# Kernel optimization log

Hardware: AMD Instinct MI355X
Metric: run time of the kernel (lower is better)

## Reference

```python
import jax, jax.numpy as jnp
import numpy as np

B, T, C = 2, 2048, 2048
NH = 16            # query heads
NKV = NH // 2      # kv heads (GQA)
HD = C // NH       # head dim = 128
N_REP = NH // NKV  # 2


def setup_inputs() -> dict:
    key = jax.random.key(0)
    k1, k2, k3 = jax.random.split(key, 3)
    x = jax.random.normal(k1, (B, T, C), jnp.float32)
    w_attn = jax.random.normal(k2, (C, (NH + 2 * NKV) * HD), jnp.float32) * 0.02
    w_proj = jax.random.normal(k3, (C, C), jnp.float32) * 0.02
    t = jnp.arange(T, dtype=jnp.float32)
    inv_freq = 1.0 / (10000.0 ** (jnp.arange(0, HD, 2, dtype=jnp.float32) / HD))
    freqs = t[:, None] * inv_freq[None, :]  # [T, HD//2]
    return {"x": x, "w_attn": w_attn, "w_proj": w_proj,
            "freqs_cos": jnp.cos(freqs), "freqs_sin": jnp.sin(freqs)}


def _rope(v, cos, sin):
    # v: [B, T, H, HD]; complex multiply on (even, odd) pairs
    vr = v.reshape(*v.shape[:-1], HD // 2, 2)
    x0, x1 = vr[..., 0], vr[..., 1]
    c = cos[None, :, None, :]
    s = sin[None, :, None, :]
    o0 = x0 * c - x1 * s
    o1 = x0 * s + x1 * c
    return jnp.stack([o0, o1], axis=-1).reshape(v.shape)


def reference(x, w_attn, w_proj, freqs_cos, freqs_sin):
    qkv = x @ w_attn  # [B, T, (NH+2*NKV)*HD]
    q, k, v = jnp.split(qkv, [NH * HD, (NH + NKV) * HD], axis=-1)
    q = q.reshape(B, T, NH, HD)
    k = k.reshape(B, T, NKV, HD)
    v = v.reshape(B, T, NKV, HD)
    q = _rope(q, freqs_cos, freqs_sin)
    k = _rope(k, freqs_cos, freqs_sin)
    # GQA: group query heads over kv heads instead of repeating k/v
    q = q.transpose(0, 2, 1, 3).reshape(B, NKV, N_REP, T, HD)  # [B, G, R, T, HD]
    k = k.transpose(0, 2, 1, 3)  # [B, G, T, HD]
    v = v.transpose(0, 2, 1, 3)  # [B, G, T, HD]
    scale = jnp.float32(1.0 / np.sqrt(HD))
    scores = jnp.einsum('bgrqd,bgkd->bgrqk', q, k) * scale
    causal = jnp.tril(jnp.ones((T, T), dtype=bool))
    scores = jnp.where(causal, scores, jnp.float32(-1e30))
    p = jax.nn.softmax(scores, axis=-1)
    y = jnp.einsum('bgrqk,bgkd->bgrqd', p, v)  # [B, G, R, T, HD]
    y = y.reshape(B, NH, T, HD).transpose(0, 2, 1, 3).reshape(B, T, C)
    return y @ w_proj
```

## Files before the change

### kernel.cpp

```cpp
#include <hip/hip_runtime.h>
#include <hip/hip_bf16.h>
#include <stdint.h>
#include <stddef.h>

typedef unsigned short u16;
using bf16x8 = __attribute__((ext_vector_type(8))) short;
using f32x4  = __attribute__((ext_vector_type(4))) float;
using f32x16 = __attribute__((ext_vector_type(16))) float;

#define DEVFN static __device__ __forceinline__

DEVFN u16 f2b(float f){ __hip_bfloat16 h = __float2bfloat16(f); return *reinterpret_cast<u16*>(&h); }
DEVFN float b2f(u16 u){ __hip_bfloat16 h; *reinterpret_cast<u16*>(&h) = u; return __bfloat162float(h); }
DEVFN uint32_t pk2(float a, float b){
  uint32_t r; asm("v_cvt_pk_bf16_f32 %0, %1, %2" : "=v"(r) : "v"(a), "v"(b)); return r;
}
DEVFN float ex2(float x){ float r; asm("v_exp_f32 %0, %1" : "=v"(r) : "v"(x)); return r; }

DEVFN void gload_lds16(const void* g, void* l){
  __builtin_amdgcn_global_load_lds(
      (const __attribute__((address_space(1))) void*)g,
      (__attribute__((address_space(3))) void*)l, 16, 0, 0);
}

__global__ void detect_k(const uint32_t* __restrict__ fc_raw, uint32_t* __restrict__ flag){
  if (threadIdx.x == 0 && blockIdx.x == 0)
    flag[0] = (fc_raw[0] == 0x3F800000u) ? 1u : 0u;
}

__global__ __launch_bounds__(256) void cvtf_k(const void* __restrict__ in, float* __restrict__ out,
                                              int n, const uint32_t* __restrict__ flag){
  const int i = blockIdx.x*256 + threadIdx.x;
  if (i >= n) return;
  if (flag[0]) out[i] = ((const float*)in)[i];
  else         out[i] = b2f(((const u16*)in)[i]);
}

__global__ __launch_bounds__(256) void cvtx_k(const void* __restrict__ in, u16* __restrict__ out,
                                              int n8, const uint32_t* __restrict__ flag){
  const int i = blockIdx.x*256 + threadIdx.x;
  if (i >= n8) return;
  __align__(16) u16 e[8];
  if (flag[0]){
    const float* f = (const float*)in + (size_t)i*8;
    float4 a = *(const float4*)f, b = *(const float4*)(f+4);
    e[0]=f2b(a.x); e[1]=f2b(a.y); e[2]=f2b(a.z); e[3]=f2b(a.w);
    e[4]=f2b(b.x); e[5]=f2b(b.y); e[6]=f2b(b.z); e[7]=f2b(b.w);
  } else {
    *(uint4*)e = *((const uint4*)in + i);
  }
  *(uint4*)(out + (size_t)i*8) = *(const uint4*)e;
}

__global__ __launch_bounds__(512) void wtrans_k(const void* __restrict__ in, u16* __restrict__ out,
                                                int C, int R, const uint32_t* __restrict__ flag){
  __shared__ __align__(16) u16 tile[64][72];
  const int r0 = blockIdx.y*64, c0 = blockIdx.x*64;
  const int t = threadIdx.x, r = t>>3, cs = (t&7)*8;
  __align__(16) u16 e[8];
  if (flag[0]){
    const float* f = (const float*)in + (size_t)(r0+r)*C + c0 + cs;
    float4 a = *(const float4*)f, b = *(const float4*)(f+4);
    e[0]=f2b(a.x); e[1]=f2b(a.y); e[2]=f2b(a.z); e[3]=f2b(a.w);
    e[4]=f2b(b.x); e[5]=f2b(b.y); e[6]=f2b(b.z); e[7]=f2b(b.w);
  } else {
    *(uint4*)e = *(const uint4*)((const u16*)in + (size_t)(r0+r)*C + c0 + cs);
  }
#pragma unroll
  for (int j=0;j<8;j++) tile[cs+j][r] = e[j];
  __syncthreads();
  uint4 o = *(const uint4*)&tile[r][cs];
  *(uint4*)(out + (size_t)(c0+r)*R + r0 + cs) = o;
}

__global__ __launch_bounds__(512) void vtrans_k(const u16* __restrict__ qkv, u16* __restrict__ vT){
  __shared__ __align__(16) u16 tile[64][72];
  const int z = blockIdx.z, b = z>>3, g = z&7;
  const u16* in = qkv + (size_t)(b*2048)*4096 + 3072 + g*128;
  u16* out = vT + (size_t)z*128*2048;
  const int r0 = blockIdx.y*64, c0 = blockIdx.x*64;
  const int t = threadIdx.x, r = t>>3, cs = (t&7)*8;
  uint4 v = *(const uint4*)(in + (size_t)(r0+r)*4096 + c0 + cs);
  const u16* e = (const u16*)&v;
#pragma unroll
  for (int j=0;j<8;j++) tile[cs+j][r] = e[j];
  __syncthreads();
  uint4 o = *(const uint4*)&tile[r][cs];
  *(uint4*)(out + (size_t)(c0+r)*2048 + r0 + cs) = o;
}

__global__ __launch_bounds__(256) void rope_k(u16* qkv, const float* __restrict__ fc,
                                              const float* __restrict__ fs){
  const int idx = blockIdx.x*256 + threadIdx.x;
  const int row = idx / 1536;
  const int p   = idx % 1536;
  const int col0 = p*2;
  const int t = row & 2047;
  const int i = p & 63;
  uint32_t* ptr = (uint32_t*)(qkv + (size_t)row*4096 + col0);
  uint32_t u = *ptr;
  float x0 = b2f((u16)(u & 0xffff));
  float x1 = b2f((u16)(u >> 16));
  float c = fc[t*64+i], s = fs[t*64+i];
  float o0 = x0*c - x1*s;
  float o1 = x0*s + x1*c;
  if (col0 < 2048){
    const float S2 = 0.08838834764831845f * 1.4426950408889634f;
    o0 *= S2; o1 *= S2;
  }
  *ptr = (uint32_t)f2b(o0) | ((uint32_t)f2b(o1) << 16);
}

__global__ __launch_bounds__(512) void gemm_p(const u16* __restrict__ A, const u16* __restrict__ Bt,
                                              void* __restrict__ Cv, int M, int N, int K,
                                              const uint32_t* __restrict__ flag, int fin){
  __shared__ __align__(16) u16 L[3*12288];
  const int nwg_x = N>>7;
  int wg = blockIdx.x;
  { const int cpx = (int)gridDim.x >> 3; wg = (wg&7)*cpx + (wg>>3); }
  const int tm = (wg / nwg_x)*256, tn = (wg % nwg_x)*128;
  const int tid = threadIdx.x, w = tid>>6, l = tid&63, lr = l&15, lg = l>>4;
  const int wm = w>>1, wn = w&1;

  f32x4 acc[4][4] = {};

  auto stage = [&](int kt, int buf){
    const int kk = kt*32;
    u16* Lb = &L[buf*12288];
#pragma unroll
    for (int j=0;j<2;j++){
      const int s = j*512 + tid;
      const int row = s>>2, c = s&3;
      const int gch = c ^ ((row ^ (row>>2)) & 3);
      gload_lds16(A + (size_t)(tm + row)*K + kk + gch*8, &Lb[(j*512 + w*64)*8]);
    }
    {
      const int s = tid;
      const int row = s>>2, c = s&3;
      const int gch = c ^ ((row ^ (row>>2)) & 3);
      gload_lds16(Bt + (size_t)(tn + row)*K + kk + gch*8, &Lb[8192 + (w*64)*8]);
    }
  };

  const int nk = K>>5;
  stage(0,0); stage(1,1);
  asm volatile("s_waitcnt vmcnt(3)" ::: "memory");
  __builtin_amdgcn_s_barrier();
  __builtin_amdgcn_sched_barrier(0);

  for (int kt=0; kt<nk; ++kt){
    const int buf = kt % 3;
    if (kt+2 < nk) stage(kt+2, (kt+2) % 3);
    const u16* Ab = &L[buf*12288];
    const u16* Bb = Ab + 8192;
    bf16x8 a[4], b[4];
#pragma unroll
    for (int mi=0;mi<4;mi++){
      const int row = wm*64 + mi*16 + lr;
      a[mi] = *(const bf16x8*)&Ab[row*32 + ((lg ^ ((row ^ (row>>2))&3))*8)];
    }
#pragma unroll
    for (int ni=0;ni<4;ni++){
      const int row = wn*64 + ni*16 + lr;
      b[ni] = *(const bf16x8*)&Bb[row*32 + ((lg ^ ((row ^ (row>>2))&3))*8)];
    }
#pragma unroll
    for (int mi=0;mi<4;mi++)
#pragma unroll
      for (int ni=0;ni<4;ni++)
        acc[mi][ni] = __builtin_amdgcn_mfma_f32_16x16x32_bf16(a[mi], b[ni], acc[mi][ni], 0,0,0);
    __builtin_amdgcn_sched_barrier(0);
    if (kt+2 < nk) asm volatile("s_waitcnt vmcnt(3)" ::: "memory");
    else           asm volatile("s_waitcnt vmcnt(0)" ::: "memory");
    __builtin_amdgcn_s_barrier();
    __builtin_amdgcn_sched_barrier(0);
  }

  const bool of32 = fin && (flag[0] != 0);
#pragma unroll
  for (int mi=0;mi<4;mi++)
#pragma unroll
    for (int ni=0;ni<4;ni++)
#pragma unroll
      for (int reg=0;reg<4;reg++){
        const int row = tm + wm*64 + mi*16 + lg*4 + reg;
        const int col = tn + wn*64 + ni*16 + lr;
        const size_t idx = (size_t)row*N + col;
        const float v = acc[mi][ni][reg];
        if (of32) ((float*)Cv)[idx] = v;
        else      ((u16*)Cv)[idx]   = f2b(v);
      }
}

__global__ __launch_bounds__(512) void gemm_p2(const u16* __restrict__ A, const u16* __restrict__ Bt,
                                               void* __restrict__ Cv, int M, int N, int K,
                                               const uint32_t* __restrict__ flag, int fin){
  __shared__ __align__(16) u16 L[3*16384];
  const int nwg_x = N>>8;
  int wg = blockIdx.x;
  { const int cpx = (int)gridDim.x >> 3; wg = (wg&7)*cpx + (wg>>3); }
  const int tm = (wg / nwg_x)*256, tn = (wg % nwg_x)*256;
  const int tid = threadIdx.x, w = tid>>6, l = tid&63, lr = l&15, lg = l>>4;
  const int wm = w>>2, wn = w&3;

  f32x4 acc[8][4] = {};

  auto stage = [&](int kt, int buf){
    const int kk = kt*32;
    u16* Lb = &L[buf*16384];
#pragma unroll
    for (int j=0;j<2;j++){
      const int s = j*512 + tid;
      const int row = s>>2, c = s&3;
      const int gch = c ^ ((row ^ (row>>2)) & 3);
      gload_lds16(A + (size_t)(tm + row)*K + kk + gch*8, &Lb[(j*512 + w*64)*8]);
    }
#pragma unroll
    for (int j=0;j<2;j++){
      const int s = j*512 + tid;
      const int row = s>>2, c = s&3;
      const int gch = c ^ ((row ^ (row>>2)) & 3);
      gload_lds16(Bt + (size_t)(tn + row)*K + kk + gch*8, &Lb[8192 + (j*512 + w*64)*8]);
    }
  };

  const int nk = K>>5;
  stage(0,0); stage(1,1);
  asm volatile("s_waitcnt vmcnt(4)" ::: "memory");
  __builtin_amdgcn_s_barrier();
  __builtin_amdgcn_sched_barrier(0);

  for (int kt=0; kt<nk; ++kt){
    const int buf = kt % 3;
    if (kt+2 < nk) stage(kt+2, (kt+2) % 3);
    const u16* Ab = &L[buf*16384];
    const u16* Bb = Ab + 8192;
    bf16x8 a[8], b[4];
#pragma unroll
    for (int mi=0;mi<8;mi++){
      const int row = wm*128 + mi*16 + lr;
      a[mi] = *(const bf16x8*)&Ab[row*32 + ((lg ^ ((row ^ (row>>2))&3))*8)];
    }
#pragma unroll
    for (int ni=0;ni<4;ni++){
      const int row = wn*64 + ni*16 + lr;
      b[ni] = *(const bf16x8*)&Bb[row*32 + ((lg ^ ((row ^ (row>>2))&3))*8)];
    }
#pragma unroll
    for (int mi=0;mi<8;mi++)
#pragma unroll
      for (int ni=0;ni<4;ni++)
        acc[mi][ni] = __builtin_amdgcn_mfma_f32_16x16x32_bf16(a[mi], b[ni], acc[mi][ni], 0,0,0);
    __builtin_amdgcn_sched_barrier(0);
    if (kt+2 < nk) asm volatile("s_waitcnt vmcnt(4)" ::: "memory");
    else           asm volatile("s_waitcnt vmcnt(0)" ::: "memory");
    __builtin_amdgcn_s_barrier();
    __builtin_amdgcn_sched_barrier(0);
  }

  const bool of32 = fin && (flag[0] != 0);
#pragma unroll
  for (int mi=0;mi<8;mi++)
#pragma unroll
    for (int ni=0;ni<4;ni++)
#pragma unroll
      for (int reg=0;reg<4;reg++){
        const int row = tm + wm*128 + mi*16 + lg*4 + reg;
        const int col = tn + wn*64 + ni*16 + lr;
        const size_t idx = (size_t)row*N + col;
        const float v = acc[mi][ni][reg];
        if (of32) ((float*)Cv)[idx] = v;
        else      ((u16*)Cv)[idx]   = f2b(v);
      }
}

__global__ __launch_bounds__(512, 1) void attn_k(const u16* __restrict__ qkv,
                                                 const u16* __restrict__ vT,
                                                 u16* __restrict__ y){
  __shared__ __align__(16) u16 KV[2][2][16384];
  const int i0 = blockIdx.x;
  const int g  = i0 & 7;
  const int r1 = i0 >> 3;
  const int hl = r1 & 1;
  const int vq = (r1 >> 1) & 7;
  const int b  = r1 >> 4;
  const int h  = g*2 + hl;

  const int tid = threadIdx.x;
  const int w = tid >> 6, l = tid & 63;
  const int grp = w >> 2, wq = w & 3;
  const int lq = l & 31;
  const int hi = l >> 5;

  const u16* kg = qkv + (size_t)(b*2048)*4096 + 2048 + g*128;
  const u16* vg = vT  + (size_t)(b*8+g)*128*2048;

  const int rk = tid >> 2, cb = tid & 3;
  uint4 kpre[4], vpre[4];
  auto loadT = [&](int kvbase){
#pragma unroll
    for (int j=0;j<4;j++){
      const int ch = cb + j*4;
      kpre[j] = *(const uint4*)(kg + (size_t)(kvbase + rk)*4096 + ch*8);
      vpre[j] = *(const uint4*)(vg + (size_t)rk*2048 + kvbase + ch*8);
    }
  };
  auto writeT = [&](int buf){
    u16* Kd = &KV[buf][rk>>6][0];
    const int rl = rk & 63;
#pragma unroll
    for (int j=0;j<4;j++){
      const int ch = cb + j*4;
      *(uint4*)&Kd[rl*128 + ((ch ^ (rl&15))*8)] = kpre[j];
    }
#pragma unroll
    for (int j=0;j<4;j++){
      const int ch = cb + j*4;
      u16* Vd = &KV[buf][ch>>3][8192];
      *(uint4*)&Vd[rk*64 + (((ch&7) ^ (rk&7))*8)] = vpre[j];
    }
  };

  int qt = vq;
  const int nA = vq + 1;
  bf16x8 qf[8];
  f32x16 yacc[4];
  float mrow, lsum;

  auto loadQ = [&]{
    const size_t qrow = (size_t)(b*2048 + qt*128 + wq*32 + lq);
    const u16* qp = qkv + qrow*4096 + h*128 + hi*8;
#pragma unroll
    for (int ds=0; ds<8; ++ds) qf[ds] = *(const bf16x8*)(qp + ds*16);
  };
  auto resetAcc = [&]{
#pragma unroll
    for (int dt=0; dt<4; ++dt)
#pragma unroll
      for (int r=0; r<16; ++r) yacc[dt][r] = 0.f;
    mrow = -1e30f; lsum = 0.f;
  };

  auto mergePhase = [&](u16* Mb){
    float* Mm = (float*)Mb; float* Ml = Mm + 128;
    u16* MOs = Mb + 512 + wq*4096;
    __syncthreads();
    if (grp == 1){
      if (l < 32){ Mm[wq*32 + l] = mrow; Ml[wq*32 + l] = lsum; }
#pragma unroll
      for (int dt=0; dt<4; ++dt)
#pragma unroll
        for (int rq=0; rq<4; ++rq){
          const int d0 = dt*32 + rq*8 + hi*4;
          uint32_t lo = pk2(yacc[dt][rq*4+0], yacc[dt][rq*4+1]);
          uint32_t hi2= pk2(yacc[dt][rq*4+2], yacc[dt][rq*4+3]);
          const int idx = (lq*128 + d0) ^ ((lq&7)<<3);
          *(uint2*)&MOs[idx] = make_uint2(lo, hi2);
        }
    }
    __syncthreads();
    if (grp == 0){
      const float mo = Mm[wq*32 + lq], lo_ = Ml[wq*32 + lq];
      const float ms = fmaxf(mrow, mo);
      const float ce = ex2(mrow - ms), co = ex2(mo - ms);
      const float inv = 1.f / (lsum*ce + lo_*co);
#pragma unroll
      for (int dt=0; dt<4; ++dt)
#pragma unroll
        for (int rq=0; rq<4; ++rq){
          const int d0 = dt*32 + rq*8 + hi*4;
          const int idx = (lq*128 + d0) ^ ((lq&7)<<3);
          uint2 pr = *(const uint2*)&MOs[idx];
          const float yo0 = b2f((u16)(pr.x & 0xffff)), yo1 = b2f((u16)(pr.x >> 16));
          const float yo2 = b2f((u16)(pr.y & 0xffff)), yo3 = b2f((u16)(pr.y >> 16));
          uint32_t lo = pk2((yacc[dt][rq*4+0]*ce + yo0*co)*inv, (yacc[dt][rq*4+1]*ce + yo1*co)*inv);
          uint32_t hi2= pk2((yacc[dt][rq*4+2]*ce + yo2*co)*inv, (yacc[dt][rq*4+3]*ce + yo3*co)*inv);
          *(uint2*)&MOs[idx] = make_uint2(lo, hi2);
        }
    }
    __syncthreads();
    const int qb2 = b*2048 + qt*128 + wq*32;
#pragma unroll
    for (int p=0; p<2; ++p){
      const int row = grp*16 + p*8 + (l>>3);
      const int gc = l & 7;
      const int idx0 = (row*128 + gc*16) ^ ((row&7)<<3);
      const int idx1 = (row*128 + gc*16 + 8) ^ ((row&7)<<3);
      uint4 v0 = *(const uint4*)&MOs[idx0];
      uint4 v1 = *(const uint4*)&MOs[idx1];
      u16* yp = y + (size_t)(qb2 + row)*2048 + h*128 + gc*16;
      *(uint4*)yp = v0;
      *(uint4*)(yp + 8) = v1;
    }
    __syncthreads();
  };

  loadT(0); writeT(0); __syncthreads();
  loadQ(); resetAcc();

  for (int s=0; s<17; ++s){
    if (s == nA){
      mergePhase(&KV[(nA&1)^1][0][0]);
      qt = 15 - vq;
      loadQ(); resetAcc();
    }
    const int sj = (s < nA) ? s : s - nA;
    const int kvbase = sj*128;
    if (s+1 < 17){
      const int s2 = s+1;
      const int sj2 = (s2 < nA) ? s2 : s2 - nA;
      loadT(sj2*128);
    }
    const u16* Kb = &KV[s&1][grp][0];
    const u16* Vb = Kb + 8192;
    const int tilebase = kvbase + grp*64;
    const int qmin = qt*128 + wq*32;
    const int qrow = qmin + lq;

    if (tilebase <= qmin + 31){
      f32x16 sc[2];
#pragma unroll
      for (int t=0;t<2;t++)
#pragma unroll
        for (int r=0;r<16;r++) sc[t][r] = 0.f;
      __builtin_amdgcn_s_setprio(1);
#pragma unroll
      for (int t=0; t<2; ++t){
        const int r = t*32 + lq;
        const int rsw = r & 15;
#pragma unroll
        for (int ds=0; ds<8; ++ds){
          const bf16x8 kf = *(const bf16x8*)&Kb[r*128 + (((2*ds+hi) ^ rsw)*8)];
          sc[t] = __builtin_amdgcn_mfma_f32_32x32x16_bf16(kf, qf[ds], sc[t], 0,0,0);
        }
      }
      __builtin_amdgcn_s_setprio(0);

      if (tilebase + 63 > qmin){
#pragma unroll
        for (int t=0;t<2;t++)
#pragma unroll
          for (int r=0;r<16;r++){
            const int kp = tilebase + t*32 + (r&3) + 8*(r>>2) + 4*hi;
            if (kp > qrow) sc[t][r] = -1e30f;
          }
      }

      float mx[16];
#pragma unroll
      for (int r=0;r<16;r++) mx[r] = fmaxf(sc[0][r], sc[1][r]);
#pragma unroll
      for (int off=8; off>0; off>>=1)
#pragma unroll
        for (int r=0;r<8;r++)
          if (r < off) mx[r] = fmaxf(mx[r], mx[r+off]);
      float pmax = fmaxf(mx[0], __shfl_xor(mx[0], 32));

      if (!__all(pmax <= mrow + 8.f)){
        const float mnew = fmaxf(mrow, pmax);
        const float corr = ex2(mrow - mnew);
        mrow = mnew; lsum *= corr;
#pragma unroll
        for (int dt=0;dt<4;dt++)
#pragma unroll
          for (int r=0;r<16;r++) yacc[dt][r] *= corr;
      }

#pragma unroll
      for (int t=0;t<2;t++)
#pragma unroll
        for (int r=0;r<16;r++) sc[t][r] = ex2(sc[t][r] - mrow);
      float sm[16];
#pragma unroll
      for (int r=0;r<16;r++) sm[r] = sc[0][r] + sc[1][r];
#pragma unroll
      for (int off=8; off>0; off>>=1)
#pragma unroll
        for (int r=0;r<8;r++)
          if (r < off) sm[r] += sm[r+off];
      lsum += sm[0] + __shfl_xor(sm[0], 32);

      __align__(16) uint32_t pw[4][4];
#pragma unroll
      for (int t=0;t<2;t++)
#pragma unroll
        for (int half=0; half<2; ++half){
          const int q8 = half*8;
          const uint32_t X0 = pk2(sc[t][q8+0], sc[t][q8+1]);
          const uint32_t X1 = pk2(sc[t][q8+2], sc[t][q8+3]);
          const uint32_t X2 = pk2(sc[t][q8+4], sc[t][q8+5]);
          const uint32_t X3 = pk2(sc[t][q8+6], sc[t][q8+7]);
          const uint32_t pX0 = (uint32_t)__shfl_xor((int)X0, 32);
          const uint32_t pX1 = (uint32_t)__shfl_xor((int)X1, 32);
          const uint32_t pX2 = (uint32_t)__shfl_xor((int)X2, 32);
          const uint32_t pX3 = (uint32_t)__shfl_xor((int)X3, 32);
          const int ks = t*2 + half;
          pw[ks][0] = hi ? pX2 : X0;
          pw[ks][1] = hi ? pX3 : X1;
          pw[ks][2] = hi ? X2 : pX0;
          pw[ks][3] = hi ? X3 : pX1;
        }

      __builtin_amdgcn_s_setprio(1);
#pragma unroll
      for (int dt=0; dt<4; ++dt){
        const int d = dt*32 + lq;
        const int dsw = d & 7;
#pragma unroll
        for (int ks=0; ks<4; ++ks){
          const bf16x8 vf = *(const bf16x8*)&Vb[d*64 + (((2*ks+hi) ^ dsw)*8)];
          yacc[dt] = __builtin_amdgcn_mfma_f32_32x32x16_bf16(vf, *(const bf16x8*)&pw[ks][0], yacc[dt], 0,0,0);
        }
      }
      __builtin_amdgcn_s_setprio(0);
    }

    if (s+1 < 17) writeT((s&1)^1);
    __syncthreads();
  }
  mergePhase(&KV[0][0][0]);
}

extern "C" void kernel_launch(void* const* d_in, const int* in_sizes, int n_in,
                              void* d_out, int out_size, void* d_ws, size_t ws_size,
                              hipStream_t stream){
  char* ws = (char*)d_ws;
  const size_t MB = 1048576;
  uint32_t* flag = (uint32_t*)(ws);
  float* fcF = (float*)(ws + 1*MB);
  float* fsF = (float*)(ws + 1*MB + 524288);
  u16* xb   = (u16*)(ws + 2*MB);
  u16* waT  = (u16*)(ws + 18*MB);
  u16* wpT  = (u16*)(ws + 34*MB);
  u16* qkvb = (u16*)(ws + 42*MB);
  u16* vTb  = (u16*)(ws + 74*MB);
  u16* yb   = xb;

  detect_k<<<1, 64, 0, stream>>>((const uint32_t*)d_in[3], flag);
  cvtf_k  <<<512, 256, 0, stream>>>(d_in[3], fcF, 131072, flag);
  cvtf_k  <<<512, 256, 0, stream>>>(d_in[4], fsF, 131072, flag);
  cvtx_k  <<<4096, 256, 0, stream>>>(d_in[0], xb, 1048576, flag);
  wtrans_k<<<dim3(64,32,1), 512, 0, stream>>>(d_in[1], waT, 4096, 2048, flag);
  wtrans_k<<<dim3(32,32,1), 512, 0, stream>>>(d_in[2], wpT, 2048, 2048, flag);
  gemm_p2 <<<dim3(256,1,1), 512, 0, stream>>>(xb, waT, qkvb, 4096, 4096, 2048, flag, 0);
  rope_k  <<<dim3(24576,1,1), 256, 0, stream>>>(qkvb, fcF, fsF);
  vtrans_k<<<dim3(2,32,16), 512, 0, stream>>>(qkvb, vTb);
  attn_k  <<<dim3(256,1,1), 512, 0, stream>>>(qkvb, vTb, yb);
  gemm_p  <<<dim3(256,1,1), 512, 0, stream>>>(yb, wpT, d_out, 4096, 2048, 2048, flag, 1);
}
```

Baseline: 260.1 us.

## Single-buffer attention K/V LDS to fit two blocks per CU

Halves the attention kernel's LDS footprint by dropping the K/V double buffer and giving the output merge its own small shared region, processed one query-wave group at a time. Launch bounds now request two 512-thread blocks per CU, aiming to hide latency through occupancy. In exchange, each KV step needs an extra barrier before overwriting the single buffer, the merge is serialized into four barrier-separated rounds, and the register budget per thread is halved, which risks spills.

```diff
diff --git a/kernel.cpp b/kernel.cpp
--- a/kernel.cpp
+++ b/kernel.cpp
@@ -274,10 +274,11 @@
       }
 }
 
-__global__ __launch_bounds__(512, 1) void attn_k(const u16* __restrict__ qkv,
+__global__ __launch_bounds__(512, 2) void attn_k(const u16* __restrict__ qkv,
                                                  const u16* __restrict__ vT,
                                                  u16* __restrict__ y){
-  __shared__ __align__(16) u16 KV[2][2][16384];
+  __shared__ __align__(16) u16 KV[2][16384];
+  __shared__ __align__(16) u16 Ms[4224];
   const int i0 = blockIdx.x;
   const int g  = i0 & 7;
   const int r1 = i0 >> 3;
@@ -305,8 +306,8 @@
       vpre[j] = *(const uint4*)(vg + (size_t)rk*2048 + kvbase + ch*8);
     }
   };
-  auto writeT = [&](int buf){
-    u16* Kd = &KV[buf][rk>>6][0];
+  auto writeT = [&](){
+    u16* Kd = &KV[rk>>6][0];
     const int rl = rk & 63;
 #pragma unroll
     for (int j=0;j<4;j++){
@@ -316,7 +317,7 @@
 #pragma unroll
     for (int j=0;j<4;j++){
       const int ch = cb + j*4;
-      u16* Vd = &KV[buf][ch>>3][8192];
+      u16* Vd = &KV[ch>>3][8192];
       *(uint4*)&Vd[rk*64 + (((ch&7) ^ (rk&7))*8)] = vpre[j];
     }
   };
@@ -341,66 +342,71 @@
     mrow = -1e30f; lsum = 0.f;
   };
 
-  auto mergePhase = [&](u16* Mb){
-    float* Mm = (float*)Mb; float* Ml = Mm + 128;
-    u16* MOs = Mb + 512 + wq*4096;
+  auto mergePhase = [&](){
+    float* Mm = (float*)Ms;
+    float* Ml = Mm + 32;
+    u16* MOs = Ms + 128;
+    for (int mq=0; mq<4; ++mq){
+      __syncthreads();
+      if (wq == mq && grp == 1){
+        if (l < 32){ Mm[l] = mrow; Ml[l] = lsum; }
+#pragma unroll
+        for (int dt=0; dt<4; ++dt)
+#pragma unroll
+          for (int rq=0; rq<4; ++rq){
+            const int d0 = dt*32 + rq*8 + hi*4;
+            uint32_t lo = pk2(yacc[dt][rq*4+0], yacc[dt][rq*4+1]);
+            uint32_t hi2= pk2(yacc[dt][rq*4+2], yacc[dt][rq*4+3]);
+            const int idx = (lq*128 + d0) ^ ((lq&7)<<3);
+            *(uint2*)&MOs[idx] = make_uint2(lo, hi2);
+          }
+      }
+      __syncthreads();
+      if (wq == mq && grp == 0){
+        const float mo = Mm[lq], lo_ = Ml[lq];
+        const float ms = fmaxf(mrow, mo);
+        const float ce = ex2(mrow - ms), co = ex2(mo - ms);
+        const float inv = 1.f / (lsum*ce + lo_*co);
+#pragma unroll
+        for (int dt=0; dt<4; ++dt)
+#pragma unroll
+          for (int rq=0; rq<4; ++rq){
+            const int d0 = dt*32 + rq*8 + hi*4;
+            const int idx = (lq*128 + d0) ^ ((lq&7)<<3);
+            uint2 pr = *(const uint2*)&MOs[idx];
+            const float yo0 = b2f((u16)(pr.x & 0xffff)), yo1 = b2f((u16)(pr.x >> 16));
+            const float yo2 = b2f((u16)(pr.y & 0xffff)), yo3 = b2f((u16)(pr.y >> 16));
+            uint32_t lo = pk2((yacc[dt][rq*4+0]*ce + yo0*co)*inv, (yacc[dt][rq*4+1]*ce + yo1*co)*inv);
+            uint32_t hi2= pk2((yacc[dt][rq*4+2]*ce + yo2*co)*inv, (yacc[dt][rq*4+3]*ce + yo3*co)*inv);
+            *(uint2*)&MOs[idx] = make_uint2(lo, hi2);
+          }
+      }
+      __syncthreads();
+      if (wq == mq){
+        const int qb2 = b*2048 + qt*128 + mq*32;
+#pragma unroll
+        for (int p=0; p<2; ++p){
+          const int row = grp*16 + p*8 + (l>>3);
+          const int gc = l & 7;
+          const int idx0 = (row*128 + gc*16) ^ ((row&7)<<3);
+          const int idx1 = (row*128 + gc*16 + 8) ^ ((row&7)<<3);
+          uint4 v0 = *(const uint4*)&MOs[idx0];
+          uint4 v1 = *(const uint4*)&MOs[idx1];
+          u16* yp = y + (size_t)(qb2 + row)*2048 + h*128 + gc*16;
+          *(uint4*)yp = v0;
+          *(uint4*)(yp + 8) = v1;
+        }
+      }
+    }
     __syncthreads();
-    if (grp == 1){
-      if (l < 32){ Mm[wq*32 + l] = mrow; Ml[wq*32 + l] = lsum; }
-#pragma unroll
-      for (int dt=0; dt<4; ++dt)
-#pragma unroll
-        for (int rq=0; rq<4; ++rq){
-          const int d0 = dt*32 + rq*8 + hi*4;
-          uint32_t lo = pk2(yacc[dt][rq*4+0], yacc[dt][rq*4+1]);
-          uint32_t hi2= pk2(yacc[dt][rq*4+2], yacc[dt][rq*4+3]);
-          const int idx = (lq*128 + d0) ^ ((lq&7)<<3);
-          *(uint2*)&MOs[idx] = make_uint2(lo, hi2);
-        }
-    }
-    __syncthreads();
-    if (grp == 0){
-      const float mo = Mm[wq*32 + lq], lo_ = Ml[wq*32 + lq];
-      const float ms = fmaxf(mrow, mo);
-      const float ce = ex2(mrow - ms), co = ex2(mo - ms);
-      const float inv = 1.f / (lsum*ce + lo_*co);
-#pragma unroll
-      for (int dt=0; dt<4; ++dt)
-#pragma unroll
-        for (int rq=0; rq<4; ++rq){
-          const int d0 = dt*32 + rq*8 + hi*4;
-          const int idx = (lq*128 + d0) ^ ((lq&7)<<3);
-          uint2 pr = *(const uint2*)&MOs[idx];
-          const float yo0 = b2f((u16)(pr.x & 0xffff)), yo1 = b2f((u16)(pr.x >> 16));
-          const float yo2 = b2f((u16)(pr.y & 0xffff)), yo3 = b2f((u16)(pr.y >> 16));
-          uint32_t lo = pk2((yacc[dt][rq*4+0]*ce + yo0*co)*inv, (yacc[dt][rq*4+1]*ce + yo1*co)*inv);
-          uint32_t hi2= pk2((yacc[dt][rq*4+2]*ce + yo2*co)*inv, (yacc[dt][rq*4+3]*ce + yo3*co)*inv);
-          *(uint2*)&MOs[idx] = make_uint2(lo, hi2);
-        }
-    }
-    __syncthreads();
-    const int qb2 = b*2048 + qt*128 + wq*32;
-#pragma unroll
-    for (int p=0; p<2; ++p){
-      const int row = grp*16 + p*8 + (l>>3);
-      const int gc = l & 7;
-      const int idx0 = (row*128 + gc*16) ^ ((row&7)<<3);
-      const int idx1 = (row*128 + gc*16 + 8) ^ ((row&7)<<3);
-      uint4 v0 = *(const uint4*)&MOs[idx0];
-      uint4 v1 = *(const uint4*)&MOs[idx1];
-      u16* yp = y + (size_t)(qb2 + row)*2048 + h*128 + gc*16;
-      *(uint4*)yp = v0;
-      *(uint4*)(yp + 8) = v1;
-    }
-    __syncthreads();
-  };
-
-  loadT(0); writeT(0); __syncthreads();
+  };
+
+  loadT(0); writeT(); __syncthreads();
   loadQ(); resetAcc();
 
   for (int s=0; s<17; ++s){
     if (s == nA){
-      mergePhase(&KV[(nA&1)^1][0][0]);
+      mergePhase();
       qt = 15 - vq;
       loadQ(); resetAcc();
     }
@@ -411,7 +417,7 @@
       const int sj2 = (s2 < nA) ? s2 : s2 - nA;
       loadT(sj2*128);
     }
-    const u16* Kb = &KV[s&1][grp][0];
+    const u16* Kb = &KV[grp][0];
     const u16* Vb = Kb + 8192;
     const int tilebase = kvbase + grp*64;
     const int qmin = qt*128 + wq*32;
@@ -515,10 +521,11 @@
       __builtin_amdgcn_s_setprio(0);
     }
 
-    if (s+1 < 17) writeT((s&1)^1);
+    __syncthreads();
+    if (s+1 < 17) writeT();
     __syncthreads();
   }
-  mergePhase(&KV[0][0][0]);
+  mergePhase();
 }
 
 extern "C" void kernel_launch(void* const* d_in, const int* in_sizes, int n_in,
```

Result: slower. 281.7 us (+8.3%).
